# Kernel tuning notes

Hardware: AMD Instinct MI355X
Metric: run time of the kernel (lower is better)

Reference implementation:

```python
import jax, jax.numpy as jnp
import numpy as np

N_NODES = 100000
IN_DIM = 128
HIDDEN = 64
N_EDGES = 1600000


def setup_inputs() -> dict:
    key = jax.random.key(0)
    k_z, k_e, k_w1, k_b1, k_w2, k_b2 = jax.random.split(key, 6)
    z = jax.random.normal(k_z, (N_NODES, IN_DIM), dtype=jnp.float32)
    edge_index = jax.random.randint(k_e, (2, N_EDGES), 0, N_NODES, dtype=jnp.int64)
    # PyTorch Linear stores weight [out, in]; keep [in, out] layout for x @ W
    bound1 = 1.0 / np.sqrt(2 * IN_DIM)
    W1 = jax.random.uniform(k_w1, (2 * IN_DIM, HIDDEN), jnp.float32, -bound1, bound1)
    b1 = jax.random.uniform(k_b1, (HIDDEN,), jnp.float32, -bound1, bound1)
    bound2 = 1.0 / np.sqrt(HIDDEN)
    W2 = jax.random.uniform(k_w2, (HIDDEN, 1), jnp.float32, -bound2, bound2)
    b2 = jax.random.uniform(k_b2, (1,), jnp.float32, -bound2, bound2)
    return {"z": z, "edge_index": edge_index, "W1": W1, "b1": b1, "W2": W2, "b2": b2}


def reference(z, edge_index, W1, b1, W2, b2):
    src = edge_index[0]
    dst = edge_index[1]
    # gather node features and concat: [E, 2*D]
    edge_feat = jnp.concatenate([z[src], z[dst]], axis=-1)
    h = jax.nn.relu(edge_feat @ W1 + b1)  # [E, H]
    logits = h @ W2 + b2                  # [E, 1]
    return jax.nn.sigmoid(logits).squeeze(-1)  # [E]
```

## Files before the change

### kernel.cpp

```cpp
#include <hip/hip_runtime.h>
#include <hip/hip_bf16.h>

#define N_NODES 100000
#define IN_DIM  128
#define HIDDEN  64
#define N_EDGES 1600000

typedef unsigned short u16;
typedef unsigned int   u32;
typedef unsigned char  u8;

typedef __attribute__((ext_vector_type(8))) short bf16x8;
typedef __attribute__((ext_vector_type(4))) float f32x4;
typedef __attribute__((ext_vector_type(2))) float f32x2;

__device__ __forceinline__ u16 f2bf(float f) {
    u32 u = __float_as_uint(f);
    u32 r = 0x7FFFu + ((u >> 16) & 1u);
    u += r;
    return (u16)(u >> 16);
}

__device__ __forceinline__ u8 f2fp8(float f) {
    u32 p = (u32)__builtin_amdgcn_cvt_pk_fp8_f32(f, f, 0, false);
    return (u8)(p & 0xFF);
}

__global__ __launch_bounds__(256) void prep_kernel(const float* __restrict__ W1,
                                                   u16* __restrict__ WcatT) {
    int idx = blockIdx.x * 256 + threadIdx.x;
    int jj = idx >> 7;
    int k  = idx & 127;
    float v = (jj < 64) ? W1[k * 64 + jj] : W1[(128 + k) * 64 + (jj - 64)];
    WcatT[idx] = f2bf(v);
}

#define LDK 136
#define GEMM_BLOCKS 625

__global__ __launch_bounds__(256) void gemm_kernel(const float* __restrict__ z,
                                                   const u16* __restrict__ WcatT,
                                                   const float* __restrict__ b1,
                                                   u8* __restrict__ UVq) {
    __shared__ u16 Bs[128 * LDK];

    int tid = threadIdx.x;
    for (int c = tid; c < 128 * 16; c += 256) {
        int row = c >> 4, cc = c & 15;
        *(uint4*)(Bs + row * LDK + cc * 8) = *(const uint4*)(WcatT + row * 128 + cc * 8);
    }
    __syncthreads();

    int wave = tid >> 6;
    int lane = tid & 63;
    int quad = lane >> 4;
    int l16  = lane & 15;

    int gwid   = blockIdx.x * 4 + wave;
    int nwaves = GEMM_BLOCKS * 4;
    const int NTILES = N_NODES / 16;

    float bias[4];
#pragma unroll
    for (int nt = 0; nt < 4; nt++) bias[nt] = b1[nt * 16 + l16];

    for (int t = gwid; t < NTILES; t += nwaves) {
        const float* zrow = z + (size_t)(t * 16 + l16) * 128;

        float4 fa[8];
#pragma unroll
        for (int kb = 0; kb < 4; kb++) {
            fa[kb * 2]     = *(const float4*)(zrow + kb * 32 + quad * 8);
            fa[kb * 2 + 1] = *(const float4*)(zrow + kb * 32 + quad * 8 + 4);
        }
        bf16x8 afrag[4];
#pragma unroll
        for (int kb = 0; kb < 4; kb++) {
            union { bf16x8 v; u32 w[4]; } pk;
            float4 lo = fa[kb * 2], hi = fa[kb * 2 + 1];
            pk.w[0] = (u32)f2bf(lo.x) | ((u32)f2bf(lo.y) << 16);
            pk.w[1] = (u32)f2bf(lo.z) | ((u32)f2bf(lo.w) << 16);
            pk.w[2] = (u32)f2bf(hi.x) | ((u32)f2bf(hi.y) << 16);
            pk.w[3] = (u32)f2bf(hi.z) | ((u32)f2bf(hi.w) << 16);
            afrag[kb] = pk.v;
        }

        f32x4 acc[8];
        const f32x4 z4 = {0.f, 0.f, 0.f, 0.f};
#pragma unroll
        for (int i = 0; i < 8; i++) acc[i] = z4;

#pragma unroll
        for (int kb = 0; kb < 4; kb++) {
            int k0 = kb * 32 + quad * 8;
#pragma unroll
            for (int nt = 0; nt < 8; nt++) {
                bf16x8 b = *(const bf16x8*)(Bs + (nt * 16 + l16) * LDK + k0);
                acc[nt] = __builtin_amdgcn_mfma_f32_16x16x32_bf16(afrag[kb], b, acc[nt], 0, 0, 0);
            }
        }

#pragma unroll
        for (int nt = 0; nt < 8; nt++) {
            float bb = (nt < 4) ? bias[nt] : 0.f;
#pragma unroll
            for (int r = 0; r < 4; r++) {
                int row = t * 16 + quad * 4 + r;
                UVq[(size_t)row * 128 + nt * 16 + l16] = f2fp8(acc[nt][r] + bb);
            }
        }
    }
}

#define BATCH 8

__global__ __launch_bounds__(256, 2) void edge_kernel(const int* __restrict__ ei,
                                                      const u8* __restrict__ UVq,
                                                      const float* __restrict__ W2,
                                                      const float* __restrict__ b2,
                                                      float* __restrict__ out) {
    int gwave = (blockIdx.x * 256 + threadIdx.x) >> 6;
    int lane  = threadIdx.x & 63;
    int sub   = lane >> 3;
    int c     = lane & 7;

    float4 w2a = *(const float4*)(W2 + c * 8);
    float4 w2b = *(const float4*)(W2 + c * 8 + 4);
    float w2r[8] = {w2a.x, w2a.y, w2a.z, w2a.w, w2b.x, w2b.y, w2b.z, w2b.w};
    float b2v = b2[0];

    int ebase = gwave * 64 + sub;

    int sB[BATCH], dB[BATCH];
#pragma unroll
    for (int j = 0; j < BATCH; j++) {
        int e = ebase + j * 8;
        sB[j] = __builtin_nontemporal_load(ei + e);
        dB[j] = __builtin_nontemporal_load(ei + N_EDGES + e);
    }
    uint2 aB[BATCH], bB[BATCH];
#pragma unroll
    for (int j = 0; j < BATCH; j++) {
        aB[j] = *(const uint2*)(UVq + (size_t)sB[j] * 128 + c * 8);
        bB[j] = *(const uint2*)(UVq + (size_t)dB[j] * 128 + 64 + c * 8);
    }
    __builtin_amdgcn_sched_barrier(0);

#pragma unroll
    for (int j = 0; j < BATCH; j++) {
        u32 aw[2] = {aB[j].x, aB[j].y};
        u32 bw[2] = {bB[j].x, bB[j].y};
        float acc = 0.f;
#pragma unroll
        for (int i = 0; i < 2; i++) {
            f32x2 uu0 = __builtin_amdgcn_cvt_pk_f32_fp8(aw[i], false);
            f32x2 vv0 = __builtin_amdgcn_cvt_pk_f32_fp8(bw[i], false);
            f32x2 uu1 = __builtin_amdgcn_cvt_pk_f32_fp8(aw[i], true);
            f32x2 vv1 = __builtin_amdgcn_cvt_pk_f32_fp8(bw[i], true);
            float h0 = fmaxf(uu0.x + vv0.x, 0.f);
            float h1 = fmaxf(uu0.y + vv0.y, 0.f);
            float h2 = fmaxf(uu1.x + vv1.x, 0.f);
            float h3 = fmaxf(uu1.y + vv1.y, 0.f);
            acc = fmaf(h0, w2r[i * 4 + 0], acc);
            acc = fmaf(h1, w2r[i * 4 + 1], acc);
            acc = fmaf(h2, w2r[i * 4 + 2], acc);
            acc = fmaf(h3, w2r[i * 4 + 3], acc);
        }
        acc += __shfl_xor(acc, 1);
        acc += __shfl_xor(acc, 2);
        acc += __shfl_xor(acc, 4);
        if (c == 0) {
            float x = acc + b2v;
            __builtin_nontemporal_store(1.f / (1.f + __expf(-x)), out + ebase + j * 8);
        }
    }
}

extern "C" void kernel_launch(void* const* d_in, const int* in_sizes, int n_in,
                              void* d_out, int out_size, void* d_ws, size_t ws_size,
                              hipStream_t stream) {
    const float* z  = (const float*)d_in[0];
    const int*   ei = (const int*)d_in[1];
    const float* W1 = (const float*)d_in[2];
    const float* b1 = (const float*)d_in[3];
    const float* W2 = (const float*)d_in[4];
    const float* b2 = (const float*)d_in[5];
    float* out = (float*)d_out;

    u16* WcatT = (u16*)d_ws;
    u8*  UVq   = (u8*)((char*)d_ws + 65536);

    prep_kernel<<<64, 256, 0, stream>>>(W1, WcatT);
    gemm_kernel<<<GEMM_BLOCKS, 256, 0, stream>>>(z, WcatT, b1, UVq);
    edge_kernel<<<6250, 256, 0, stream>>>(ei, UVq, W2, b2, out);
}
```

Before: 152.5 us.

## Widen edge gathers to 16B per lane and pack fp8 stores in GEMM

In the GEMM, the MFMA operands are swapped so each lane holds four consecutive output columns of one row. That lets the bias be added with a float4 and four fp8 values be packed into a single 32-bit store instead of four byte stores. The z loads become nontemporal. In the edge kernel, each edge is handled by 4 lanes loading 16 bytes each instead of 8 lanes loading 8 bytes, which halves the block count and removes one shuffle step. The per-lane register count and ILP per lane rise in exchange.

```diff
diff --git a/kernel.cpp b/kernel.cpp
--- a/kernel.cpp
+++ b/kernel.cpp
@@ -19,11 +19,6 @@
     u32 r = 0x7FFFu + ((u >> 16) & 1u);
     u += r;
     return (u16)(u >> 16);
-}
-
-__device__ __forceinline__ u8 f2fp8(float f) {
-    u32 p = (u32)__builtin_amdgcn_cvt_pk_fp8_f32(f, f, 0, false);
-    return (u8)(p & 0xFF);
 }
 
 __global__ __launch_bounds__(256) void prep_kernel(const float* __restrict__ W1,
@@ -60,28 +55,28 @@
     int nwaves = GEMM_BLOCKS * 4;
     const int NTILES = N_NODES / 16;
 
-    float bias[4];
+    float4 bias4[4];
 #pragma unroll
-    for (int nt = 0; nt < 4; nt++) bias[nt] = b1[nt * 16 + l16];
+    for (int nt = 0; nt < 4; nt++) bias4[nt] = *(const float4*)(b1 + nt * 16 + quad * 4);
 
     for (int t = gwid; t < NTILES; t += nwaves) {
         const float* zrow = z + (size_t)(t * 16 + l16) * 128;
 
-        float4 fa[8];
+        f32x4 fa[8];
 #pragma unroll
         for (int kb = 0; kb < 4; kb++) {
-            fa[kb * 2]     = *(const float4*)(zrow + kb * 32 + quad * 8);
-            fa[kb * 2 + 1] = *(const float4*)(zrow + kb * 32 + quad * 8 + 4);
+            fa[kb * 2]     = __builtin_nontemporal_load((const f32x4*)(zrow + kb * 32 + quad * 8));
+            fa[kb * 2 + 1] = __builtin_nontemporal_load((const f32x4*)(zrow + kb * 32 + quad * 8 + 4));
         }
         bf16x8 afrag[4];
 #pragma unroll
         for (int kb = 0; kb < 4; kb++) {
             union { bf16x8 v; u32 w[4]; } pk;
-            float4 lo = fa[kb * 2], hi = fa[kb * 2 + 1];
-            pk.w[0] = (u32)f2bf(lo.x) | ((u32)f2bf(lo.y) << 16);
-            pk.w[1] = (u32)f2bf(lo.z) | ((u32)f2bf(lo.w) << 16);
-            pk.w[2] = (u32)f2bf(hi.x) | ((u32)f2bf(hi.y) << 16);
-            pk.w[3] = (u32)f2bf(hi.z) | ((u32)f2bf(hi.w) << 16);
+            f32x4 lo = fa[kb * 2], hi = fa[kb * 2 + 1];
+            pk.w[0] = (u32)f2bf(lo[0]) | ((u32)f2bf(lo[1]) << 16);
+            pk.w[1] = (u32)f2bf(lo[2]) | ((u32)f2bf(lo[3]) << 16);
+            pk.w[2] = (u32)f2bf(hi[0]) | ((u32)f2bf(hi[1]) << 16);
+            pk.w[3] = (u32)f2bf(hi[2]) | ((u32)f2bf(hi[3]) << 16);
             afrag[kb] = pk.v;
         }
 
@@ -95,24 +90,27 @@
             int k0 = kb * 32 + quad * 8;
 #pragma unroll
             for (int nt = 0; nt < 8; nt++) {
-                bf16x8 b = *(const bf16x8*)(Bs + (nt * 16 + l16) * LDK + k0);
-                acc[nt] = __builtin_amdgcn_mfma_f32_16x16x32_bf16(afrag[kb], b, acc[nt], 0, 0, 0);
+                bf16x8 bw = *(const bf16x8*)(Bs + (nt * 16 + l16) * LDK + k0);
+                acc[nt] = __builtin_amdgcn_mfma_f32_16x16x32_bf16(bw, afrag[kb], acc[nt], 0, 0, 0);
             }
         }
 
+        u8* orow = UVq + (size_t)(t * 16 + l16) * 128;
 #pragma unroll
         for (int nt = 0; nt < 8; nt++) {
-            float bb = (nt < 4) ? bias[nt] : 0.f;
-#pragma unroll
-            for (int r = 0; r < 4; r++) {
-                int row = t * 16 + quad * 4 + r;
-                UVq[(size_t)row * 128 + nt * 16 + l16] = f2fp8(acc[nt][r] + bb);
+            float x0 = acc[nt][0], x1 = acc[nt][1], x2 = acc[nt][2], x3 = acc[nt][3];
+            if (nt < 4) {
+                x0 += bias4[nt].x; x1 += bias4[nt].y; x2 += bias4[nt].z; x3 += bias4[nt].w;
             }
+            u32 w = (u32)__builtin_amdgcn_cvt_pk_fp8_f32(x0, x1, 0, false);
+            w = (u32)__builtin_amdgcn_cvt_pk_fp8_f32(x2, x3, (int)w, true);
+            *(u32*)(orow + nt * 16 + quad * 4) = w;
         }
     }
 }
 
 #define BATCH 8
+#define EDGE_BLOCKS 3125
 
 __global__ __launch_bounds__(256, 2) void edge_kernel(const int* __restrict__ ei,
                                                       const u8* __restrict__ UVq,
@@ -121,38 +119,42 @@
                                                       float* __restrict__ out) {
     int gwave = (blockIdx.x * 256 + threadIdx.x) >> 6;
     int lane  = threadIdx.x & 63;
-    int sub   = lane >> 3;
-    int c     = lane & 7;
+    int sub   = lane >> 2;
+    int c     = lane & 3;
 
-    float4 w2a = *(const float4*)(W2 + c * 8);
-    float4 w2b = *(const float4*)(W2 + c * 8 + 4);
-    float w2r[8] = {w2a.x, w2a.y, w2a.z, w2a.w, w2b.x, w2b.y, w2b.z, w2b.w};
+    float w2r[16];
+#pragma unroll
+    for (int q = 0; q < 4; q++) {
+        float4 t4 = *(const float4*)(W2 + c * 16 + q * 4);
+        w2r[q * 4 + 0] = t4.x; w2r[q * 4 + 1] = t4.y;
+        w2r[q * 4 + 2] = t4.z; w2r[q * 4 + 3] = t4.w;
+    }
     float b2v = b2[0];
 
-    int ebase = gwave * 64 + sub;
+    int ebase = gwave * 128 + sub;
 
     int sB[BATCH], dB[BATCH];
 #pragma unroll
     for (int j = 0; j < BATCH; j++) {
-        int e = ebase + j * 8;
+        int e = ebase + j * 16;
         sB[j] = __builtin_nontemporal_load(ei + e);
         dB[j] = __builtin_nontemporal_load(ei + N_EDGES + e);
     }
-    uint2 aB[BATCH], bB[BATCH];
+    uint4 aB[BATCH], bB[BATCH];
 #pragma unroll
     for (int j = 0; j < BATCH; j++) {
-        aB[j] = *(const uint2*)(UVq + (size_t)sB[j] * 128 + c * 8);
-        bB[j] = *(const uint2*)(UVq + (size_t)dB[j] * 128 + 64 + c * 8);
+        aB[j] = *(const uint4*)(UVq + (size_t)sB[j] * 128 + c * 16);
+        bB[j] = *(const uint4*)(UVq + (size_t)dB[j] * 128 + 64 + c * 16);
     }
     __builtin_amdgcn_sched_barrier(0);
 
 #pragma unroll
     for (int j = 0; j < BATCH; j++) {
-        u32 aw[2] = {aB[j].x, aB[j].y};
-        u32 bw[2] = {bB[j].x, bB[j].y};
+        u32 aw[4] = {aB[j].x, aB[j].y, aB[j].z, aB[j].w};
+        u32 bw[4] = {bB[j].x, bB[j].y, bB[j].z, bB[j].w};
         float acc = 0.f;
 #pragma unroll
-        for (int i = 0; i < 2; i++) {
+        for (int i = 0; i < 4; i++) {
             f32x2 uu0 = __builtin_amdgcn_cvt_pk_f32_fp8(aw[i], false);
             f32x2 vv0 = __builtin_amdgcn_cvt_pk_f32_fp8(bw[i], false);
             f32x2 uu1 = __builtin_amdgcn_cvt_pk_f32_fp8(aw[i], true);
@@ -168,10 +170,9 @@
         }
         acc += __shfl_xor(acc, 1);
         acc += __shfl_xor(acc, 2);
-        acc += __shfl_xor(acc, 4);
         if (c == 0) {
             float x = acc + b2v;
-            __builtin_nontemporal_store(1.f / (1.f + __expf(-x)), out + ebase + j * 8);
+            __builtin_nontemporal_store(1.f / (1.f + __expf(-x)), out + ebase + j * 16);
         }
     }
 }
@@ -192,5 +193,5 @@
 
     prep_kernel<<<64, 256, 0, stream>>>(W1, WcatT);
     gemm_kernel<<<GEMM_BLOCKS, 256, 0, stream>>>(z, WcatT, b1, UVq);
-    edge_kernel<<<6250, 256, 0, stream>>>(ei, UVq, W2, b2, out);
+    edge_kernel<<<EDGE_BLOCKS, 256, 0, stream>>>(ei, UVq, W2, b2, out);
 }
```

New measurement: 158.6 us. 4.0% more time.
